# Optimization experiments

Measured on AMD Instinct MI355X. Metric: run time of the kernel, lower is better.

The kernel has to match this reference:

```python
import jax, jax.numpy as jnp
import numpy as np

N = 100000     # nodes
H = 128        # hidden_channels == in_channels
OUT = 64       # out_channels
L = 3          # num_layers=4 -> num_layers-1 Layer modules
E = 1_600_000  # unique undirected edges (avg degree 16)
BN_EPS = 1e-5


def _make_edges():
    # Unique undirected edges, no self-loops -> dense symmetric adjacency in the
    # original module is exactly this edge set symmetrized.
    rng = np.random.default_rng(0)
    i = rng.integers(0, N, 1_700_000)
    j = rng.integers(0, N, 1_700_000)
    m = i != j
    i, j = i[m], j[m]
    lo, hi = np.minimum(i, j), np.maximum(i, j)
    pairs = np.unique(lo.astype(np.int64) * N + hi)[:E]
    lo = (pairs // N).astype(np.int32)
    hi = (pairs % N).astype(np.int32)
    src = jnp.asarray(np.concatenate([lo, hi]))  # [2E] directed
    dst = jnp.asarray(np.concatenate([hi, lo]))
    return src, dst


def setup_inputs() -> dict:
    key = jax.random.key(0)
    ks = jax.random.split(key, 24)
    nrm = lambda k, s: (jax.random.normal(k, s, dtype=jnp.float32) * 0.05)
    src, dst = _make_edges()
    return {
        "x": jax.random.normal(ks[0], (N, H), dtype=jnp.float32),
        "src": src,
        "dst": dst,
        # per-Layer MLP(in=H, hidden=H, out=H): Linear->ReLU->Linear, stacked over L
        "layer_W1": nrm(ks[1], (L, H, H)),
        "layer_b1": nrm(ks[2], (L, H)),
        "layer_W2": nrm(ks[3], (L, H, H)),
        "layer_b2": nrm(ks[4], (L, H)),
        # BatchNorm1d (eval mode: running stats)
        "bn_gamma": 1.0 + nrm(ks[5], (L, H)),
        "bn_beta": nrm(ks[6], (L, H)),
        "bn_mean": nrm(ks[7], (L, H)),
        "bn_var": jax.random.uniform(ks[8], (L, H), jnp.float32, 0.5, 1.5),
        # single shared GRUCell(H, H)
        "gru_Wih": nrm(ks[9], (3 * H, H)),
        "gru_Whh": nrm(ks[10], (3 * H, H)),
        "gru_bih": nrm(ks[11], (3 * H,)),
        "gru_bhh": nrm(ks[12], (3 * H,)),
        # mlp_last: MLP(H, H, OUT)
        "last_W1": nrm(ks[13], (H, H)),
        "last_b1": nrm(ks[14], (H,)),
        "last_W2": nrm(ks[15], (OUT, H)),
        "last_b2": nrm(ks[16], (OUT,)),
    }


def reference(x, src, dst, layer_W1, layer_b1, layer_W2, layer_b2,
              bn_gamma, bn_beta, bn_mean, bn_var,
              gru_Wih, gru_Whh, gru_bih, gru_bhh,
              last_W1, last_b1, last_W2, last_b2):
    n = x.shape[0]
    deg = jax.ops.segment_sum(jnp.ones(src.shape[0], x.dtype), dst, num_segments=n)
    inv_deg = (1.0 / jnp.maximum(deg, 1.0))[:, None]  # isolated nodes -> 0 agg
    h = jnp.zeros((n, H), x.dtype)
    for l in range(L):
        agg = jax.ops.segment_sum(x[src], dst, num_segments=n) * inv_deg  # mean over neighbors
        c = x + agg
        c = jnp.maximum(c @ layer_W1[l].T + layer_b1[l], 0.0) @ layer_W2[l].T + layer_b2[l]
        c = bn_gamma[l] * (c - bn_mean[l]) * jax.lax.rsqrt(bn_var[l] + BN_EPS) + bn_beta[l]
        # F.dropout(training=False) is identity
        gi = c @ gru_Wih.T + gru_bih  # [n, 3H]
        gh = h @ gru_Whh.T + gru_bhh
        r = jax.nn.sigmoid(gi[:, :H] + gh[:, :H])
        z = jax.nn.sigmoid(gi[:, H:2 * H] + gh[:, H:2 * H])
        nst = jnp.tanh(gi[:, 2 * H:] + r * gh[:, 2 * H:])
        h = (1.0 - z) * nst + z * h
        x = h
    return jnp.maximum(x @ last_W1.T + last_b1, 0.0) @ last_W2.T + last_b2
```

## Files before the change

### kernel.cpp

```cpp
#include <hip/hip_runtime.h>
#include <hip/hip_bf16.h>
#include <stdint.h>

typedef __bf16 bf16;
typedef __bf16 bf16x8 __attribute__((ext_vector_type(8)));
typedef float f32x4 __attribute__((ext_vector_type(4)));
typedef float f32x2 __attribute__((ext_vector_type(2)));
typedef uint32_t u32x4 __attribute__((ext_vector_type(4)));

#define HD 128
#define LDP (HD + 8)
#define NTPB 4
#define MFMA __builtin_amdgcn_mfma_f32_16x16x32_bf16

__device__ inline float bflo(uint32_t u){ return __uint_as_float(u << 16); }
__device__ inline float bfhi(uint32_t u){ return __uint_as_float(u & 0xffff0000u); }
__device__ inline uint32_t packbf(float a, float b){
    bf16 x = (bf16)a, y = (bf16)b;
    uint16_t ux = __builtin_bit_cast(uint16_t, x), uy = __builtin_bit_cast(uint16_t, y);
    return (uint32_t)ux | ((uint32_t)uy << 16);
}
__device__ inline bf16x8 ldb8(const bf16* p){ return *(const bf16x8*)p; }
__device__ inline float sigm(float x){ return 1.f / (1.f + __expf(-x)); }
__device__ inline float tanh_fast(float x){ float t = __expf(-2.f * x); return (1.f - t) / (1.f + t); }
__device__ inline uint32_t swz(uint32_t b){ return b ^ (((b >> 8) & 7u) << 4); }

__global__ void k_cvt(const float* __restrict__ in, bf16* __restrict__ out, int n){
    int i = blockIdx.x * 256 + threadIdx.x;
    if (i < n) out[i] = (bf16)in[i];
}

__global__ void k_cvt_x(const float* __restrict__ in, uint32_t* __restrict__ out, int nU){
    int i = blockIdx.x * 256 + threadIdx.x;
    if (i >= nU) return;
    int r = i >> 6, dw = i & 63;
    uint32_t v = packbf(in[(size_t)i * 2], in[(size_t)i * 2 + 1]);
    int slot = dw >> 2, w = dw & 3;
    out[(size_t)r * 64 + (((slot ^ (r & 7)) << 2) | w)] = v;
}

__global__ void k_bound(const int* __restrict__ dstB, int E, int* __restrict__ rows2, int n){
    int v = blockIdx.x * 256 + threadIdx.x;
    if (v > n) return;
    int lo = 0, hi = E;
    while (lo < hi){ int mid = (lo + hi) >> 1; if (dstB[mid] < v) lo = mid + 1; else hi = mid; }
    rows2[v] = lo;
}

__global__ void k_count(const int* __restrict__ dst, int* __restrict__ deg, int ne){
    int i = blockIdx.x * 256 + threadIdx.x;
    if (i < ne) atomicAdd(&deg[dst[i]], 1);
}

__global__ void k_scan1(const int* __restrict__ deg, int* __restrict__ rows,
                        int* __restrict__ bsum, int n){
    __shared__ int lds[256];
    int b = blockIdx.x, tid = threadIdx.x;
    int i0 = b * 1024 + tid * 4;
    int v[4]; int s = 0;
#pragma unroll
    for (int j = 0; j < 4; ++j){ int idx = i0 + j; v[j] = (idx < n) ? deg[idx] : 0; s += v[j]; }
    lds[tid] = s; __syncthreads();
    int acc = s;
    for (int off = 1; off < 256; off <<= 1){
        int add = (tid >= off) ? lds[tid - off] : 0;
        __syncthreads();
        acc += add; lds[tid] = acc;
        __syncthreads();
    }
    int run = acc - s;
#pragma unroll
    for (int j = 0; j < 4; ++j){ int idx = i0 + j; if (idx < n) rows[idx] = run; run += v[j]; }
    if (tid == 255) bsum[b] = acc;
}

__global__ void k_scan2(int* __restrict__ bsum, int nb){
    __shared__ int lds[128];
    int tid = threadIdx.x;
    int v = (tid < nb) ? bsum[tid] : 0;
    lds[tid] = v; __syncthreads();
    int acc = v;
    for (int off = 1; off < 128; off <<= 1){
        int add = (tid >= off) ? lds[tid - off] : 0;
        __syncthreads();
        acc += add; lds[tid] = acc;
        __syncthreads();
    }
    if (tid < nb) bsum[tid] = acc - v;
}

__global__ void k_scan3(int* __restrict__ rows, const int* __restrict__ bsum, int n, int total){
    int i = blockIdx.x * 256 + threadIdx.x;
    if (i < n) rows[i] += bsum[i >> 10];
    if (i == n) rows[n] = total;
}

__global__ void k_fillp(const int* __restrict__ src, const int* __restrict__ dst,
                        int* __restrict__ cur, int* __restrict__ col, int ne, int nPerG){
    int g = blockIdx.x & 7;
    int i = (blockIdx.x >> 3) * 256 + threadIdx.x;
    if (i >= ne) return;
    int d = dst[i];
    int lo = g * nPerG;
    if (d >= lo && d < lo + nPerG){
        int p = atomicAdd(&cur[d], 1);
        col[p] = src[i];
    }
}

__global__ __launch_bounds__(256) void k_gather(
    const bf16* __restrict__ curx,
    const int* __restrict__ srcB, const int* __restrict__ rows2,
    const int* __restrict__ colB, const int* __restrict__ rowsB,
    bf16* __restrict__ cout, int n)
{
    int wid = threadIdx.x >> 6, lane = threadIdx.x & 63;
    int v = blockIdx.x * 4 + wid;
    if (v >= n) return;
    int grp = lane >> 3, sl = lane & 7;
    int a0 = rows2[v], a1 = rows2[v + 1];
    int b0 = rowsB[v], b1 = rowsB[v + 1];
    int deg = (a1 - a0) + (b1 - b0);
    float inv = (deg > 0) ? 1.f / (float)deg : 0.f;

    const u32x4* base = (const u32x4*)curx;
    f32x2 acc2[8];
#pragma unroll
    for (int k = 0; k < 8; ++k) acc2[k] = (f32x2){0.f, 0.f};

    for (int j = a0 + grp; j < a1; j += 8){
        int nb = srcB[j];
        int px = nb & 7;
        u32x4 q0 = base[(size_t)nb * 16 + (sl ^ px)];
        u32x4 q1 = base[(size_t)nb * 16 + 8 + (sl ^ px)];
#pragma unroll
        for (int k = 0; k < 4; ++k){
            acc2[k]     += (f32x2){bflo(q0[k]), bfhi(q0[k])};
            acc2[4 + k] += (f32x2){bflo(q1[k]), bfhi(q1[k])};
        }
    }
    for (int j = b0 + grp; j < b1; j += 8){
        int nb = colB[j];
        int px = nb & 7;
        u32x4 q0 = base[(size_t)nb * 16 + (sl ^ px)];
        u32x4 q1 = base[(size_t)nb * 16 + 8 + (sl ^ px)];
#pragma unroll
        for (int k = 0; k < 4; ++k){
            acc2[k]     += (f32x2){bflo(q0[k]), bfhi(q0[k])};
            acc2[4 + k] += (f32x2){bflo(q1[k]), bfhi(q1[k])};
        }
    }
    float acc[16];
#pragma unroll
    for (int k = 0; k < 4; ++k){
        acc[2*k]     = acc2[k].x;     acc[2*k+1]     = acc2[k].y;
        acc[8+2*k]   = acc2[4+k].x;   acc[8+2*k+1]   = acc2[4+k].y;
    }
#pragma unroll
    for (int k = 0; k < 16; ++k){
        acc[k] += __shfl_xor(acc[k], 8);
        acc[k] += __shfl_xor(acc[k], 16);
        acc[k] += __shfl_xor(acc[k], 32);
    }
    if (grp == 0){
        int pv = v & 7;
        u32x4 x0 = base[(size_t)v * 16 + (sl ^ pv)];
        u32x4 x1 = base[(size_t)v * 16 + 8 + (sl ^ pv)];
        u32x4 o0, o1;
#pragma unroll
        for (int k = 0; k < 4; ++k){
            o0[k] = packbf(bflo(x0[k]) + acc[2*k] * inv,   bfhi(x0[k]) + acc[2*k+1] * inv);
            o1[k] = packbf(bflo(x1[k]) + acc[8+2*k] * inv, bfhi(x1[k]) + acc[8+2*k+1] * inv);
        }
        ((u32x4*)cout)[(size_t)v * 16 + (sl ^ pv)]     = o0;
        ((u32x4*)cout)[(size_t)v * 16 + 8 + (sl ^ pv)] = o1;
    }
}

#define MT_C0 0u
#define MT_C1 16384u
#define MT_A  32768u
__global__ __launch_bounds__(512, 4) void k_mlp(
    const bf16* __restrict__ cin, bf16* __restrict__ cbn,
    const bf16* __restrict__ W1, const float* __restrict__ b1,
    const bf16* __restrict__ W2, const float* __restrict__ b2,
    const float* __restrict__ gm, const float* __restrict__ bt,
    const float* __restrict__ mu, const float* __restrict__ vr, int nT)
{
    __shared__ __align__(16) char smem[49152];
    int tid = threadIdx.x, wid = tid >> 6, lane = tid & 63;
    int rA = lane & 15, u = lane >> 4, ko = u * 8;
    int c = wid * 16 + rA;

    bf16x8 W1f[4], W2f[4];
#pragma unroll
    for (int kk = 0; kk < 4; ++kk){
        W1f[kk] = ldb8(W1 + (size_t)c * HD + ko + kk * 32);
        W2f[kk] = ldb8(W2 + (size_t)c * HD + ko + kk * 32);
    }
    float b1c = b1[c];
    float bnS = gm[c] * rsqrtf(vr[c] + 1e-5f);
    float bnO = bt[c] - mu[c] * bnS;
    float b2c = b2[c];

    auto gload = [&](const char* g, uint32_t lo){
        __builtin_amdgcn_global_load_lds(
            (const __attribute__((address_space(1))) void*)g,
            (__attribute__((address_space(3))) void*)(smem + lo), 16, 0, 0);
    };
    auto stageC = [&](int t, uint32_t dst){
        const char* g = (const char*)cin + (size_t)t * 16384 + (size_t)lane * 16;
#pragma unroll
        for (int i = 0; i < 2; ++i){
            uint32_t ch = (uint32_t)(wid * 2 + i) * 1024;
            gload(g + ch, dst + ch);
        }
    };

    int t = blockIdx.x;
    int cur = 0;
    if (t < nT) stageC(t, MT_C0);
    asm volatile("s_waitcnt vmcnt(0) lgkmcnt(0)" ::: "memory");
    __builtin_amdgcn_sched_barrier(0);
    __builtin_amdgcn_s_barrier();

    for (; t < nT; t += (int)gridDim.x){
        int tn = t + (int)gridDim.x;
        if (tn < nT) stageC(tn, cur ? MT_C0 : MT_C1);
        uint32_t CB = cur ? MT_C1 : MT_C0;

#pragma unroll
        for (int m = 0; m < 4; ++m){
            bf16x8 a_[4];
#pragma unroll
            for (int kk = 0; kk < 4; ++kk){
                uint32_t b = (uint32_t)(m * 16 + rA) * 256 + (uint32_t)(u * 16 + kk * 64);
                a_[kk] = *(const bf16x8*)(smem + CB + swz(b));
            }
            f32x4 acc = {0,0,0,0};
#pragma unroll
            for (int kk = 0; kk < 4; ++kk) acc = MFMA(a_[kk], W1f[kk], acc, 0, 0, 0);
#pragma unroll
            for (int j = 0; j < 4; ++j){
                uint32_t r = (uint32_t)(m * 16 + u * 4 + j);
                *(bf16*)(smem + MT_A + swz(r * 256 + (uint32_t)c * 2)) =
                    (bf16)fmaxf(acc[j] + b1c, 0.f);
            }
        }
        asm volatile("s_waitcnt lgkmcnt(0)" ::: "memory");
        __builtin_amdgcn_sched_barrier(0);
        __builtin_amdgcn_s_barrier();

#pragma unroll
        for (int m = 0; m < 4; ++m){
            bf16x8 a_[4];
#pragma unroll
            for (int kk = 0; kk < 4; ++kk){
                uint32_t b = (uint32_t)(m * 16 + rA) * 256 + (uint32_t)(u * 16 + kk * 64);
                a_[kk] = *(const bf16x8*)(smem + MT_A + swz(b));
            }
            f32x4 acc = {0,0,0,0};
#pragma unroll
            for (int kk = 0; kk < 4; ++kk) acc = MFMA(a_[kk], W2f[kk], acc, 0, 0, 0);
#pragma unroll
            for (int j = 0; j < 4; ++j){
                uint32_t r = (uint32_t)(m * 16 + u * 4 + j);
                *(bf16*)(smem + CB + swz(r * 256 + (uint32_t)c * 2)) =
                    (bf16)((acc[j] + b2c) * bnS + bnO);
            }
        }
        asm volatile("s_waitcnt lgkmcnt(0)" ::: "memory");
        __builtin_amdgcn_sched_barrier(0);
        __builtin_amdgcn_s_barrier();

        {
            char* gout = (char*)cbn + (size_t)t * 16384;
#pragma unroll
            for (int i = 0; i < 2; ++i){
                uint32_t off = (uint32_t)tid * 16 + (uint32_t)i * 8192;
                *(u32x4*)(gout + off) = *(const u32x4*)(smem + CB + off);
            }
        }
        asm volatile("s_waitcnt vmcnt(2) lgkmcnt(0)" ::: "memory");
        __builtin_amdgcn_sched_barrier(0);
        __builtin_amdgcn_s_barrier();
        cur ^= 1;
    }
}

#define GT_C0 0u
#define GT_C1 24576u
#define GT_H0 49152u
#define GT_H1 73728u
#define GT_O  98304u
__global__ __launch_bounds__(512, 1) void k_gru(
    const bf16* __restrict__ cbn, const bf16* __restrict__ hOld, bf16* __restrict__ hNew,
    const bf16* __restrict__ Wih, const bf16* __restrict__ Whh,
    const float* __restrict__ bih, const float* __restrict__ bhh, int nT)
{
    __shared__ __align__(16) char smem[122880];
    int tid = threadIdx.x, wid = tid >> 6, lane = tid & 63;
    int rA = lane & 15, u = lane >> 4, ko = u * 8;
    int c = wid * 16 + rA;

    bf16x8 Gri[4], Grh[4], Gzi[4], Gzh[4], Gni[4], Gnh[4];
#pragma unroll
    for (int kk = 0; kk < 4; ++kk){
        Gri[kk] = ldb8(Wih + (size_t)c * HD + ko + kk * 32);
        Gzi[kk] = ldb8(Wih + (size_t)(c + 128) * HD + ko + kk * 32);
        Gni[kk] = ldb8(Wih + (size_t)(c + 256) * HD + ko + kk * 32);
        Grh[kk] = ldb8(Whh + (size_t)c * HD + ko + kk * 32);
        Gzh[kk] = ldb8(Whh + (size_t)(c + 128) * HD + ko + kk * 32);
        Gnh[kk] = ldb8(Whh + (size_t)(c + 256) * HD + ko + kk * 32);
    }
    float br = bih[c] + bhh[c], bz = bih[c + 128] + bhh[c + 128];
    float bin = bih[c + 256], bhn = bhh[c + 256];

    auto gload = [&](const char* g, uint32_t lo){
        __builtin_amdgcn_global_load_lds(
            (const __attribute__((address_space(1))) void*)g,
            (__attribute__((address_space(3))) void*)(smem + lo), 16, 0, 0);
    };
    auto stageC = [&](int t, uint32_t dst){
        const char* g = (const char*)cbn + (size_t)t * 24576 + (size_t)lane * 16;
#pragma unroll
        for (int i = 0; i < 3; ++i){
            uint32_t ch = (uint32_t)(wid * 3 + i) * 1024;
            gload(g + ch, dst + ch);
        }
    };
    auto stageH = [&](int t, uint32_t dst){
        const char* g = (const char*)hOld + (size_t)t * 24576 + (size_t)lane * 16;
#pragma unroll
        for (int i = 0; i < 3; ++i){
            uint32_t ch = (uint32_t)(wid * 3 + i) * 1024;
            gload(g + ch, dst + ch);
        }
    };

    int t = blockIdx.x;
    int cur = 0;
    if (t < nT){ stageC(t, GT_C0); stageH(t, GT_H0); }
    asm volatile("s_waitcnt vmcnt(0) lgkmcnt(0)" ::: "memory");
    __builtin_amdgcn_sched_barrier(0);
    __builtin_amdgcn_s_barrier();

    for (; t < nT; t += (int)gridDim.x){
        int tn = t + (int)gridDim.x;
        if (tn < nT){
            stageC(tn, cur ? GT_C0 : GT_C1);
            stageH(tn, cur ? GT_H0 : GT_H1);
        }
        uint32_t CB = cur ? GT_C1 : GT_C0;
        uint32_t HB = cur ? GT_H1 : GT_H0;

#pragma unroll
        for (int m = 0; m < 6; ++m){
            bf16x8 ac_[4], ah_[4];
#pragma unroll
            for (int kk = 0; kk < 4; ++kk){
                uint32_t b = (uint32_t)(m * 16 + rA) * 256 + (uint32_t)(u * 16 + kk * 64);
                ac_[kk] = *(const bf16x8*)(smem + CB + swz(b));
                ah_[kk] = *(const bf16x8*)(smem + HB + swz(b));
            }
            f32x4 rr = {0,0,0,0}, zz = {0,0,0,0}, gi = {0,0,0,0}, gh = {0,0,0,0};
#pragma unroll
            for (int kk = 0; kk < 4; ++kk){
                rr = MFMA(ac_[kk], Gri[kk], rr, 0, 0, 0);
                rr = MFMA(ah_[kk], Grh[kk], rr, 0, 0, 0);
                zz = MFMA(ac_[kk], Gzi[kk], zz, 0, 0, 0);
                zz = MFMA(ah_[kk], Gzh[kk], zz, 0, 0, 0);
                gi = MFMA(ac_[kk], Gni[kk], gi, 0, 0, 0);
                gh = MFMA(ah_[kk], Gnh[kk], gh, 0, 0, 0);
            }
#pragma unroll
            for (int j = 0; j < 4; ++j){
                uint32_t r = (uint32_t)(m * 16 + u * 4 + j);
                uint32_t inner = swz(r * 256 + (uint32_t)c * 2);
                float hold = (float)*(const bf16*)(smem + HB + inner);
                float rg = sigm(rr[j] + br);
                float zg = sigm(zz[j] + bz);
                float ng = tanh_fast(gi[j] + bin + rg * (gh[j] + bhn));
                *(bf16*)(smem + GT_O + inner) = (bf16)((1.f - zg) * ng + zg * hold);
            }
        }
        asm volatile("s_waitcnt lgkmcnt(0)" ::: "memory");
        __builtin_amdgcn_sched_barrier(0);
        __builtin_amdgcn_s_barrier();

        {
            char* hNb = (char*)hNew + (size_t)t * 24576;
#pragma unroll
            for (int i = 0; i < 3; ++i){
                uint32_t off = (uint32_t)tid * 16 + (uint32_t)i * 8192;
                *(u32x4*)(hNb + off) = *(const u32x4*)(smem + GT_O + off);
            }
        }
        asm volatile("s_waitcnt vmcnt(3) lgkmcnt(0)" ::: "memory");
        __builtin_amdgcn_sched_barrier(0);
        __builtin_amdgcn_s_barrier();
        cur ^= 1;
    }
}

__global__ __launch_bounds__(256) void k_final(
    const bf16* __restrict__ hin, const bf16* __restrict__ W1, const float* __restrict__ b1,
    const bf16* __restrict__ W2, const float* __restrict__ b2,
    float* __restrict__ out, int nTiles)
{
    __shared__ bf16 lds[NTPB][16][LDP];
    int wid = threadIdx.x >> 6, lane = threadIdx.x & 63;
    int tile = blockIdx.x * NTPB + wid;
    if (tile >= nTiles) return;
    int r0 = tile * 16;
    int rA = lane & 15, u = lane >> 4, ko = u * 8;

    bf16x8 a[4];
    const char* hb = (const char*)hin;
    uint32_t b0 = (uint32_t)(r0 + rA) * 256 + (uint32_t)(u * 16);
#pragma unroll
    for (int kk = 0; kk < 4; ++kk) a[kk] = *(const bf16x8*)(hb + swz(b0 + (uint32_t)kk * 64));

#pragma unroll
    for (int t = 0; t < 8; ++t){
        f32x4 acc = {0.f, 0.f, 0.f, 0.f};
        int c = t * 16 + rA;
        const bf16* bp = W1 + (size_t)c * HD + ko;
#pragma unroll
        for (int kk = 0; kk < 4; ++kk)
            acc = MFMA(a[kk], ldb8(bp + kk * 32), acc, 0, 0, 0);
        float bias = b1[c];
#pragma unroll
        for (int j = 0; j < 4; ++j){
            float v = fmaxf(acc[j] + bias, 0.f);
            lds[wid][u * 4 + j][c] = (bf16)v;
        }
    }
    __threadfence_block();
    bf16x8 a2[4];
    const bf16* lp = &lds[wid][rA][ko];
#pragma unroll
    for (int kk = 0; kk < 4; ++kk) a2[kk] = ldb8(lp + kk * 32);

#pragma unroll
    for (int t = 0; t < 4; ++t){
        f32x4 acc = {0.f, 0.f, 0.f, 0.f};
        int c = t * 16 + rA;
        const bf16* bp = W2 + (size_t)c * HD + ko;
#pragma unroll
        for (int kk = 0; kk < 4; ++kk)
            acc = MFMA(a2[kk], ldb8(bp + kk * 32), acc, 0, 0, 0);
        float bias = b2[c];
#pragma unroll
        for (int j = 0; j < 4; ++j)
            out[(size_t)(r0 + u * 4 + j) * 64 + c] = acc[j] + bias;
    }
}

extern "C" void kernel_launch(void* const* d_in, const int* in_sizes, int n_in,
                              void* d_out, int out_size, void* d_ws, size_t ws_size,
                              hipStream_t stream)
{
    const float* x    = (const float*)d_in[0];
    const int*   src  = (const int*)d_in[1];
    const int*   dst  = (const int*)d_in[2];
    const float* lW1  = (const float*)d_in[3];
    const float* lb1  = (const float*)d_in[4];
    const float* lW2  = (const float*)d_in[5];
    const float* lb2  = (const float*)d_in[6];
    const float* gmm  = (const float*)d_in[7];
    const float* bta  = (const float*)d_in[8];
    const float* mun  = (const float*)d_in[9];
    const float* vrr  = (const float*)d_in[10];
    const float* Wih  = (const float*)d_in[11];
    const float* Whh  = (const float*)d_in[12];
    const float* bih  = (const float*)d_in[13];
    const float* bhh  = (const float*)d_in[14];
    const float* fW1  = (const float*)d_in[15];
    const float* fb1  = (const float*)d_in[16];
    const float* fW2  = (const float*)d_in[17];
    const float* fb2  = (const float*)d_in[18];

    int n  = in_sizes[0] / HD;
    int ne = in_sizes[1];
    int E  = ne / 2;
    int L  = in_sizes[3] / (HD * HD);
    int nPad = (n + 191) / 192 * 192;

    char* w = (char*)d_ws;
    auto alloc = [&](size_t bytes) -> char* {
        char* p = w; w += (bytes + 255) & ~(size_t)255; return p;
    };
    bf16* xbf  = (bf16*)alloc((size_t)nPad * HD * 2);
    bf16* hA   = (bf16*)alloc((size_t)nPad * HD * 2);
    bf16* hB   = (bf16*)alloc((size_t)nPad * HD * 2);
    bf16* cin  = (bf16*)alloc((size_t)nPad * HD * 2);
    bf16* cbn  = (bf16*)alloc((size_t)nPad * HD * 2);
    bf16* W1b  = (bf16*)alloc((size_t)L * HD * HD * 2);
    bf16* W2b  = (bf16*)alloc((size_t)L * HD * HD * 2);
    bf16* Wib  = (bf16*)alloc((size_t)3 * HD * HD * 2);
    bf16* Whb  = (bf16*)alloc((size_t)3 * HD * HD * 2);
    bf16* fW1b = (bf16*)alloc((size_t)HD * HD * 2);
    bf16* fW2b = (bf16*)alloc((size_t)64 * HD * 2);
    int*  degB = (int*)alloc((size_t)n * 4);
    int*  rowsB= (int*)alloc((size_t)(n + 1) * 4);
    int*  rows2= (int*)alloc((size_t)(n + 1) * 4);
    int*  bsum = (int*)alloc(512);
    int*  curB = (int*)alloc((size_t)n * 4);
    int*  colB = (int*)alloc((size_t)E * 4);

    auto cvt = [&](const float* i, bf16* o, int cnt){
        k_cvt<<<(cnt + 255) / 256, 256, 0, stream>>>(i, o, cnt);
    };
    int nU = n * 64;
    k_cvt_x<<<(nU + 255) / 256, 256, 0, stream>>>(x, (uint32_t*)xbf, nU);
    cvt(lW1, W1b,  L * HD * HD);
    cvt(lW2, W2b,  L * HD * HD);
    cvt(Wih, Wib,  3 * HD * HD);
    cvt(Whh, Whb,  3 * HD * HD);
    cvt(fW1, fW1b, HD * HD);
    cvt(fW2, fW2b, 64 * HD);

    hipMemsetAsync(degB, 0, (size_t)n * 4, stream);
    hipMemsetAsync(hA, 0, (size_t)nPad * HD * 2, stream);

    k_bound<<<(n + 1 + 255) / 256, 256, 0, stream>>>(dst + E, E, rows2, n);
    k_count<<<(E + 255) / 256, 256, 0, stream>>>(dst, degB, E);
    int nb = (n + 1023) / 1024;
    k_scan1<<<nb, 256, 0, stream>>>(degB, rowsB, bsum, n);
    k_scan2<<<1, 128, 0, stream>>>(bsum, nb);
    k_scan3<<<(n + 1 + 255) / 256, 256, 0, stream>>>(rowsB, bsum, n, E);
    hipMemcpyAsync(curB, rowsB, (size_t)n * 4, hipMemcpyDeviceToDevice, stream);
    int nPerG = (n + 7) / 8;
    k_fillp<<<8 * ((E + 255) / 256), 256, 0, stream>>>(src, dst, curB, colB, E, nPerG);

    int nT64 = nPad / 64;
    int nT96 = nPad / 96;
    int gM = (nT64 < 512) ? nT64 : 512;
    int gG = (nT96 < 256) ? nT96 : 256;
    int nT16 = (n + 15) / 16;
    int gF = (nT16 + NTPB - 1) / NTPB;

    const bf16* curp = xbf;
    for (int l = 0; l < L; ++l){
        k_gather<<<(n + 3) / 4, 256, 0, stream>>>(curp, src + E, rows2, colB, rowsB, cin, n);
        k_mlp<<<gM, 512, 0, stream>>>(cin, cbn,
            W1b + (size_t)l * HD * HD, lb1 + l * HD,
            W2b + (size_t)l * HD * HD, lb2 + l * HD,
            gmm + l * HD, bta + l * HD, mun + l * HD, vrr + l * HD, nT64);
        k_gru<<<gG, 512, 0, stream>>>(cbn, hA, hB, Wib, Whb, bih, bhh, nT96);
        bf16* tmp = hA; hA = hB; hB = tmp;
        curp = hA;
    }
    k_final<<<gF, 256, 0, stream>>>(hA, fW1b, fb1, fW2b, fb2, (float*)d_out, nT16);
}
```

Baseline: 748.0 us.

## Merge setup launches and software-pipeline neighbor loads in gather

Six weight-conversion launches become one segmented conversion kernel. The binary-search bound and degree count kernels merge into one launch. The curB copy is folded into the scan fixup kernel, removing several launches and a memcpy. The gather loop now unifies the two edge ranges into one loop and prefetches the next neighbor row while accumulating the current one, raising memory-level parallelism at the cost of more registers.

```diff
diff --git a/kernel.cpp b/kernel.cpp
--- a/kernel.cpp
+++ b/kernel.cpp
@@ -25,9 +25,18 @@
 __device__ inline float tanh_fast(float x){ float t = __expf(-2.f * x); return (1.f - t) / (1.f + t); }
 __device__ inline uint32_t swz(uint32_t b){ return b ^ (((b >> 8) & 7u) << 4); }
 
-__global__ void k_cvt(const float* __restrict__ in, bf16* __restrict__ out, int n){
+struct CvtSeg { const float* s; bf16* d; };
+struct Cvt6 { CvtSeg seg[6]; int cum[7]; };
+__global__ void k_cvt6(Cvt6 a, int total){
     int i = blockIdx.x * 256 + threadIdx.x;
-    if (i < n) out[i] = (bf16)in[i];
+    if (i >= total) return;
+#pragma unroll
+    for (int s = 0; s < 6; ++s){
+        if (i >= a.cum[s] && i < a.cum[s + 1]){
+            int k = i - a.cum[s];
+            a.seg[s].d[k] = (bf16)a.seg[s].s[k];
+        }
+    }
 }
 
 __global__ void k_cvt_x(const float* __restrict__ in, uint32_t* __restrict__ out, int nU){
@@ -39,17 +48,18 @@
     out[(size_t)r * 64 + (((slot ^ (r & 7)) << 2) | w)] = v;
 }
 
-__global__ void k_bound(const int* __restrict__ dstB, int E, int* __restrict__ rows2, int n){
-    int v = blockIdx.x * 256 + threadIdx.x;
-    if (v > n) return;
-    int lo = 0, hi = E;
-    while (lo < hi){ int mid = (lo + hi) >> 1; if (dstB[mid] < v) lo = mid + 1; else hi = mid; }
-    rows2[v] = lo;
-}
-
-__global__ void k_count(const int* __restrict__ dst, int* __restrict__ deg, int ne){
-    int i = blockIdx.x * 256 + threadIdx.x;
-    if (i < ne) atomicAdd(&deg[dst[i]], 1);
+__global__ void k_bc(const int* __restrict__ dstB, int E, int* __restrict__ rows2, int n,
+                     const int* __restrict__ dst, int* __restrict__ deg, int nbB){
+    if ((int)blockIdx.x < nbB){
+        int v = blockIdx.x * 256 + threadIdx.x;
+        if (v > n) return;
+        int lo = 0, hi = E;
+        while (lo < hi){ int mid = (lo + hi) >> 1; if (dstB[mid] < v) lo = mid + 1; else hi = mid; }
+        rows2[v] = lo;
+    } else {
+        int i = (blockIdx.x - nbB) * 256 + threadIdx.x;
+        if (i < E) atomicAdd(&deg[dst[i]], 1);
+    }
 }
 
 __global__ void k_scan1(const int* __restrict__ deg, int* __restrict__ rows,
@@ -89,9 +99,10 @@
     if (tid < nb) bsum[tid] = acc - v;
 }
 
-__global__ void k_scan3(int* __restrict__ rows, const int* __restrict__ bsum, int n, int total){
+__global__ void k_scan3(int* __restrict__ rows, const int* __restrict__ bsum,
+                        int* __restrict__ curB, int n, int total){
     int i = blockIdx.x * 256 + threadIdx.x;
-    if (i < n) rows[i] += bsum[i >> 10];
+    if (i < n){ int r = rows[i] + bsum[i >> 10]; rows[i] = r; curB[i] = r; }
     if (i == n) rows[n] = total;
 }
 
@@ -120,36 +131,43 @@
     int grp = lane >> 3, sl = lane & 7;
     int a0 = rows2[v], a1 = rows2[v + 1];
     int b0 = rowsB[v], b1 = rowsB[v + 1];
-    int deg = (a1 - a0) + (b1 - b0);
-    float inv = (deg > 0) ? 1.f / (float)deg : 0.f;
+    int lenA = a1 - a0;
+    int tot  = lenA + (b1 - b0);
+    float inv = (tot > 0) ? 1.f / (float)tot : 0.f;
 
     const u32x4* base = (const u32x4*)curx;
     f32x2 acc2[8];
 #pragma unroll
     for (int k = 0; k < 8; ++k) acc2[k] = (f32x2){0.f, 0.f};
 
-    for (int j = a0 + grp; j < a1; j += 8){
-        int nb = srcB[j];
-        int px = nb & 7;
-        u32x4 q0 = base[(size_t)nb * 16 + (sl ^ px)];
-        u32x4 q1 = base[(size_t)nb * 16 + 8 + (sl ^ px)];
+    auto nbidx = [&](int p)->int {
+        return (p < lenA) ? srcB[a0 + p] : colB[b0 + p - lenA];
+    };
+
+    u32x4 qa0, qa1;
+    int p = grp;
+    if (p < tot){
+        int nb = nbidx(p); int px = nb & 7;
+        qa0 = base[(size_t)nb * 16 + (sl ^ px)];
+        qa1 = base[(size_t)nb * 16 + 8 + (sl ^ px)];
+    }
+    while (p < tot){
+        int pn = p + 8;
+        u32x4 qb0, qb1;
+        if (pn < tot){
+            int nb = nbidx(pn); int px = nb & 7;
+            qb0 = base[(size_t)nb * 16 + (sl ^ px)];
+            qb1 = base[(size_t)nb * 16 + 8 + (sl ^ px)];
+        }
 #pragma unroll
         for (int k = 0; k < 4; ++k){
-            acc2[k]     += (f32x2){bflo(q0[k]), bfhi(q0[k])};
-            acc2[4 + k] += (f32x2){bflo(q1[k]), bfhi(q1[k])};
-        }
-    }
-    for (int j = b0 + grp; j < b1; j += 8){
-        int nb = colB[j];
-        int px = nb & 7;
-        u32x4 q0 = base[(size_t)nb * 16 + (sl ^ px)];
-        u32x4 q1 = base[(size_t)nb * 16 + 8 + (sl ^ px)];
-#pragma unroll
-        for (int k = 0; k < 4; ++k){
-            acc2[k]     += (f32x2){bflo(q0[k]), bfhi(q0[k])};
-            acc2[4 + k] += (f32x2){bflo(q1[k]), bfhi(q1[k])};
-        }
-    }
+            acc2[k]     += (f32x2){bflo(qa0[k]), bfhi(qa0[k])};
+            acc2[4 + k] += (f32x2){bflo(qa1[k]), bfhi(qa1[k])};
+        }
+        qa0 = qb0; qa1 = qb1;
+        p = pn;
+    }
+
     float acc[16];
 #pragma unroll
     for (int k = 0; k < 4; ++k){
@@ -509,28 +527,33 @@
     int*  curB = (int*)alloc((size_t)n * 4);
     int*  colB = (int*)alloc((size_t)E * 4);
 
-    auto cvt = [&](const float* i, bf16* o, int cnt){
-        k_cvt<<<(cnt + 255) / 256, 256, 0, stream>>>(i, o, cnt);
-    };
     int nU = n * 64;
     k_cvt_x<<<(nU + 255) / 256, 256, 0, stream>>>(x, (uint32_t*)xbf, nU);
-    cvt(lW1, W1b,  L * HD * HD);
-    cvt(lW2, W2b,  L * HD * HD);
-    cvt(Wih, Wib,  3 * HD * HD);
-    cvt(Whh, Whb,  3 * HD * HD);
-    cvt(fW1, fW1b, HD * HD);
-    cvt(fW2, fW2b, 64 * HD);
+
+    {
+        Cvt6 a;
+        int LHH = L * HD * HD, G = 3 * HD * HD, F1 = HD * HD, F2 = 64 * HD;
+        a.seg[0] = {lW1, W1b};  a.seg[1] = {lW2, W2b};
+        a.seg[2] = {Wih, Wib};  a.seg[3] = {Whh, Whb};
+        a.seg[4] = {fW1, fW1b}; a.seg[5] = {fW2, fW2b};
+        a.cum[0] = 0;
+        a.cum[1] = LHH;         a.cum[2] = LHH * 2;
+        a.cum[3] = LHH * 2 + G; a.cum[4] = LHH * 2 + G * 2;
+        a.cum[5] = a.cum[4] + F1; a.cum[6] = a.cum[5] + F2;
+        int total = a.cum[6];
+        k_cvt6<<<(total + 255) / 256, 256, 0, stream>>>(a, total);
+    }
 
     hipMemsetAsync(degB, 0, (size_t)n * 4, stream);
     hipMemsetAsync(hA, 0, (size_t)nPad * HD * 2, stream);
 
-    k_bound<<<(n + 1 + 255) / 256, 256, 0, stream>>>(dst + E, E, rows2, n);
-    k_count<<<(E + 255) / 256, 256, 0, stream>>>(dst, degB, E);
+    int nbB = (n + 1 + 255) / 256;
+    int nbC = (E + 255) / 256;
+    k_bc<<<nbB + nbC, 256, 0, stream>>>(dst + E, E, rows2, n, dst, degB, nbB);
     int nb = (n + 1023) / 1024;
     k_scan1<<<nb, 256, 0, stream>>>(degB, rowsB, bsum, n);
     k_scan2<<<1, 128, 0, stream>>>(bsum, nb);
-    k_scan3<<<(n + 1 + 255) / 256, 256, 0, stream>>>(rowsB, bsum, n, E);
-    hipMemcpyAsync(curB, rowsB, (size_t)n * 4, hipMemcpyDeviceToDevice, stream);
+    k_scan3<<<(n + 1 + 255) / 256, 256, 0, stream>>>(rowsB, bsum, curB, n, E);
     int nPerG = (n + 7) / 8;
     k_fillp<<<8 * ((E + 255) / 256), 256, 0, stream>>>(src, dst, curB, colB, E, nPerG);
 
```

Measured after the change: 729.2 us. 1.03x faster.
